# Performance work log

Measured on AMD Instinct MI355X. Metric: run time of the kernel, lower is better.

## Reference

```python
import jax, jax.numpy as jnp
import numpy as np

N_NODES = 100000
N_EDGES = 1600000
IN_F, HID_F, OUT_F = 128, 128, 64


def _sage_conv(x, src, dst, W_self, W_neigh, b, n_nodes):
    # DGL SAGEConv 'mean': out = x @ W_self + mean_{u in N(v)} x_u @ W_neigh + b
    agg = jax.ops.segment_sum(x[src], dst, num_segments=n_nodes)  # [N, d]
    deg = jax.ops.segment_sum(jnp.ones_like(dst, dtype=x.dtype), dst, num_segments=n_nodes)
    neigh = agg / jnp.maximum(deg, 1.0)[:, None]  # zero-in-degree nodes -> 0
    return x @ W_self + neigh @ W_neigh + b


def setup_inputs() -> dict:
    key = jax.random.key(0)
    ks = jax.random.split(key, 8)
    return {
        "features": jax.random.normal(ks[0], (N_NODES, IN_F), dtype=jnp.float32),
        "edge_src": jax.random.randint(ks[1], (N_EDGES,), 0, N_NODES, dtype=jnp.int32),
        "edge_dst": jax.random.randint(ks[2], (N_EDGES,), 0, N_NODES, dtype=jnp.int32),
        "W1_self": jax.random.normal(ks[3], (IN_F, HID_F), dtype=jnp.float32) / np.sqrt(IN_F),
        "W1_neigh": jax.random.normal(ks[4], (IN_F, HID_F), dtype=jnp.float32) / np.sqrt(IN_F),
        "b1": jnp.zeros((HID_F,), dtype=jnp.float32),
        "W2_self": jax.random.normal(ks[5], (HID_F, OUT_F), dtype=jnp.float32) / np.sqrt(HID_F),
        "W2_neigh": jax.random.normal(ks[6], (HID_F, OUT_F), dtype=jnp.float32) / np.sqrt(HID_F),
        "b2": jnp.zeros((OUT_F,), dtype=jnp.float32),
    }


def reference(features, edge_src, edge_dst, W1_self, W1_neigh, b1, W2_self, W2_neigh, b2):
    n = features.shape[0]
    x = _sage_conv(features, edge_src, edge_dst, W1_self, W1_neigh, b1, n)
    x = jax.nn.relu(x)
    # dropout with training=False is a no-op
    return _sage_conv(x, edge_src, edge_dst, W2_self, W2_neigh, b2, n)
```

## Files before the change

kernel.cpp:

```cpp
#include <hip/hip_runtime.h>

#define NODES 100000
#define EDGES 1600000
#define BSH 8
#define NBUCK ((NODES + 255) >> BSH)
#define CHUNK 4096
#define LMAX 8192
#define MCHUNKS ((NODES + 31) / 32)
#define CONVB 12500

using bf16x8 = __attribute__((ext_vector_type(8))) short;
using f32x4  = __attribute__((ext_vector_type(4))) float;
using f32x2  = __attribute__((ext_vector_type(2))) float;

__device__ __forceinline__ unsigned short f2b(float f) {
    unsigned u = __builtin_bit_cast(unsigned, f);
    unsigned r = (u + 0x7FFFu + ((u >> 16) & 1u)) >> 16;
    return (unsigned short)r;
}

__device__ __forceinline__ f32x2 pkadd(f32x2 a, f32x2 b) {
    f32x2 d;
    asm("v_pk_add_f32 %0, %1, %2" : "=v"(d) : "v"(a), "v"(b));
    return d;
}
__device__ __forceinline__ f32x2 pkfma(f32x2 a, f32x2 b, f32x2 c) {
    f32x2 d;
    asm("v_pk_fma_f32 %0, %1, %2, %3" : "=v"(d) : "v"(a), "v"(b), "v"(c));
    return d;
}
__device__ __forceinline__ unsigned cvt2bf(float lo, float hi) {
    unsigned r;
    asm("v_cvt_pk_bf16_f32 %0, %1, %2" : "=v"(r) : "v"(lo), "v"(hi));
    return r;
}

__device__ __forceinline__ void addpk8(f32x2* a, uint2 v) {
    a[0] = pkadd(a[0], __builtin_amdgcn_cvt_pk_f32_fp8((int)v.x, false));
    a[1] = pkadd(a[1], __builtin_amdgcn_cvt_pk_f32_fp8((int)v.x, true));
    a[2] = pkadd(a[2], __builtin_amdgcn_cvt_pk_f32_fp8((int)v.y, false));
    a[3] = pkadd(a[3], __builtin_amdgcn_cvt_pk_f32_fp8((int)v.y, true));
}


__global__ __launch_bounds__(256) void conv_hist(
    const float* __restrict__ in, unsigned short* __restrict__ outb,
    unsigned char* __restrict__ outq, int n4,
    const float* __restrict__ W1s, const float* __restrict__ W1n,
    const float* __restrict__ W2s, const float* __restrict__ W2n,
    unsigned short* __restrict__ Wt1s, unsigned short* __restrict__ Wt1n,
    unsigned short* __restrict__ Wt2s, unsigned short* __restrict__ Wt2n,
    const int* __restrict__ dst, int* __restrict__ bucket_cnt) {
    int t = threadIdx.x;
    if (blockIdx.x < CONVB) {
        int i = blockIdx.x * 256 + t;
        if (i < n4) {
            float4 v = reinterpret_cast<const float4*>(in)[i];
            uint2 o;
            o.x = (unsigned)f2b(v.x) | ((unsigned)f2b(v.y) << 16);
            o.y = (unsigned)f2b(v.z) | ((unsigned)f2b(v.w) << 16);
            reinterpret_cast<uint2*>(outb)[i] = o;
            int pk = __builtin_amdgcn_cvt_pk_fp8_f32(v.x, v.y, 0, false);
            pk = __builtin_amdgcn_cvt_pk_fp8_f32(v.z, v.w, pk, true);
            reinterpret_cast<unsigned*>(outq)[i] = (unsigned)pk;
        }
        if (i < 16384) {
            int k = i >> 7, n = i & 127;
            Wt1s[n * 128 + k] = f2b(W1s[i]);
            Wt1n[n * 128 + k] = f2b(W1n[i]);
        }
        if (i < 8192) {
            int k = i >> 6, n = i & 63;
            Wt2s[n * 128 + k] = f2b(W2s[i]);
            Wt2n[n * 128 + k] = f2b(W2n[i]);
        }
        return;
    }
    __shared__ int lcnt[512];
    lcnt[t] = 0; lcnt[t + 256] = 0;
    __syncthreads();
    int base = (blockIdx.x - CONVB) * 16384;
    int n = EDGES - base;
    if (n > 16384) n = 16384;
    const int4* d4 = reinterpret_cast<const int4*>(dst + base);
    for (int i = t; i < (n >> 2); i += 256) {
        int4 d = d4[i];
        atomicAdd(&lcnt[d.x >> BSH], 1);
        atomicAdd(&lcnt[d.y >> BSH], 1);
        atomicAdd(&lcnt[d.z >> BSH], 1);
        atomicAdd(&lcnt[d.w >> BSH], 1);
    }
    for (int i = (n & ~3) + t; i < n; i += 256) atomicAdd(&lcnt[dst[base + i] >> BSH], 1);
    __syncthreads();
    if (lcnt[t]) atomicAdd(&bucket_cnt[t], lcnt[t]);
    if (lcnt[t + 256]) atomicAdd(&bucket_cnt[t + 256], lcnt[t + 256]);
}

__global__ void bscan_kernel(const int* __restrict__ bucket_cnt, int* __restrict__ bucket_off,
                             int* __restrict__ gcursor, int* __restrict__ row_ptr) {
    __shared__ int sh[512];
    int t = threadIdx.x;
    int v = (t < NBUCK) ? bucket_cnt[t] : 0;
    sh[t] = v;
    __syncthreads();
    for (int off = 1; off < 512; off <<= 1) {
        int x = (t >= off) ? sh[t - off] : 0;
        __syncthreads();
        sh[t] += x;
        __syncthreads();
    }
    int excl = sh[t] - v;
    if (t < NBUCK) { bucket_off[t] = excl; gcursor[t] = excl; }
    if (t == NBUCK) bucket_off[t] = EDGES;
    if (t == 0) row_ptr[NODES] = EDGES;
}

__global__ __launch_bounds__(256) void binscat_kernel(
    const int* __restrict__ src, const int* __restrict__ dst,
    int* __restrict__ gcursor, unsigned* __restrict__ pairs) {
    __shared__ int cnt[512];
    __shared__ int scn[512];
    __shared__ int gbs[512];
    __shared__ int cur[512];
    __shared__ uint2 stage[CHUNK];
    int t = threadIdx.x;
    int base = blockIdx.x * CHUNK;
    int n = EDGES - base;
    if (n > CHUNK) n = CHUNK;

    cnt[t] = 0; cnt[t + 256] = 0;
    __syncthreads();

    uint2 my[16];
#pragma unroll
    for (int i = 0; i < 16; ++i) {
        int idx = t + i * 256;
        if (idx < n) {
            int d = dst[base + idx];
            int s = src[base + idx];
            my[i] = make_uint2((unsigned)d, (unsigned)s);
            atomicAdd(&cnt[d >> BSH], 1);
        } else {
            my[i] = make_uint2(0xFFFFFFFFu, 0);
        }
    }
    __syncthreads();
    scn[t] = cnt[t]; scn[t + 256] = cnt[t + 256];
    __syncthreads();
    for (int off = 1; off < 512; off <<= 1) {
        int a0 = (t >= off) ? scn[t - off] : 0;
        int a1 = (t + 256 >= off) ? scn[t + 256 - off] : 0;
        __syncthreads();
        scn[t] += a0; scn[t + 256] += a1;
        __syncthreads();
    }
    cur[t] = scn[t] - cnt[t];
    cur[t + 256] = scn[t + 256] - cnt[t + 256];
    __syncthreads();
#pragma unroll
    for (int i = 0; i < 16; ++i) {
        if (my[i].x != 0xFFFFFFFFu) {
            int b = (int)(my[i].x >> BSH);
            int p = atomicAdd(&cur[b], 1);
            stage[p] = my[i];
        }
    }
    for (int b2 = t; b2 < 512; b2 += 256) {
        int c = cnt[b2];
        gbs[b2] = (c > 0 && b2 < NBUCK) ? atomicAdd(&gcursor[b2], c) : 0;
    }
    __syncthreads();
    for (int idx = t; idx < n; idx += 256) {
        uint2 p = stage[idx];
        int b = (int)(p.x >> BSH);
        int excl = scn[b] - cnt[b];
        pairs[gbs[b] + idx - excl] = ((p.x & 255u) << 24) | p.y;
    }
}

__global__ __launch_bounds__(256) void localsort_kernel(
    const unsigned* __restrict__ pairs, const int* __restrict__ bucket_off,
    int* __restrict__ row_ptr, int* __restrict__ src_sorted) {
    __shared__ int cnt[256];
    __shared__ int cur[256];
    __shared__ int stage[LMAX];
    int b = blockIdx.x;
    int t = threadIdx.x;
    int node0 = b << BSH;
    int pbeg = bucket_off[b], pend = bucket_off[b + 1];
    int n = pend - pbeg;
    cnt[t] = 0;
    __syncthreads();
    for (int e = pbeg + t; e < pend; e += 256)
        atomicAdd(&cnt[(int)(pairs[e] >> 24)], 1);
    __syncthreads();
    int v = cnt[t];
    cur[t] = v;
    __syncthreads();
    for (int off = 1; off < 256; off <<= 1) {
        int x = (t >= off) ? cur[t - off] : 0;
        __syncthreads();
        cur[t] += x;
        __syncthreads();
    }
    int excl = cur[t] - v;
    int node = node0 + t;
    if (node < NODES) row_ptr[node] = pbeg + excl;
    cur[t] = excl;
    __syncthreads();
    if (n <= LMAX) {
        for (int e = pbeg + t; e < pend; e += 256) {
            unsigned p = pairs[e];
            int pos = atomicAdd(&cur[(int)(p >> 24)], 1);
            stage[pos] = (int)(p & 0xFFFFFFu);
        }
        __syncthreads();
        for (int i = t; i < n; i += 256) src_sorted[pbeg + i] = stage[i];
    } else {
        for (int e = pbeg + t; e < pend; e += 256) {
            unsigned p = pairs[e];
            int pos = atomicAdd(&cur[(int)(p >> 24)], 1);
            src_sorted[pbeg + pos] = (int)(p & 0xFFFFFFu);
        }
    }
}


__global__ __launch_bounds__(256) void agg128_fp8(
    const unsigned char* __restrict__ xq, const int* __restrict__ row_ptr,
    const int* __restrict__ srcs, unsigned short* __restrict__ out) {
    int wave = (blockIdx.x * 256 + threadIdx.x) >> 6;
    int lane = threadIdx.x & 63;
    int sl = lane & 15;
    int n = wave * 4 + (lane >> 4);
    if (n >= NODES) return;
    int beg = row_ptr[n], end = row_ptr[n + 1];
    int gb = lane & 48;

    f32x2 A0[4], A1[4];
#pragma unroll
    for (int i = 0; i < 4; ++i) { A0[i] = {0.f, 0.f}; A1[i] = {0.f, 0.f}; }

    const unsigned char* xs = xq + sl * 8;
    for (int base = beg; base < end; base += 16) {
        int idx = base + sl;
        int sv = (idx < end) ? srcs[idx] : NODES;
        uint2 vv[8], ww[8];
#pragma unroll
        for (int j = 0; j < 8; ++j) {
            int s = __shfl(sv, gb + j, 64);
            vv[j] = *reinterpret_cast<const uint2*>(xs + (size_t)s * 128);
        }
#pragma unroll
        for (int j = 0; j < 8; ++j) {
            int s = __shfl(sv, gb + 8 + j, 64);
            ww[j] = *reinterpret_cast<const uint2*>(xs + (size_t)s * 128);
        }
#pragma unroll
        for (int j = 0; j < 8; ++j) addpk8((j & 1) ? A1 : A0, vv[j]);
#pragma unroll
        for (int j = 0; j < 8; ++j) addpk8((j & 1) ? A0 : A1, ww[j]);
    }

    float inv = 1.0f / fmaxf((float)(end - beg), 1.0f);
    f32x2 iv = {inv, inv};
    f32x2 z = {0.f, 0.f};
    f32x2 r0 = pkfma(pkadd(A0[0], A1[0]), iv, z);
    f32x2 r1 = pkfma(pkadd(A0[1], A1[1]), iv, z);
    f32x2 r2 = pkfma(pkadd(A0[2], A1[2]), iv, z);
    f32x2 r3 = pkfma(pkadd(A0[3], A1[3]), iv, z);
    uint4 o;
    o.x = cvt2bf(r0[0], r0[1]);
    o.y = cvt2bf(r1[0], r1[1]);
    o.z = cvt2bf(r2[0], r2[1]);
    o.w = cvt2bf(r3[0], r3[1]);
    *reinterpret_cast<uint4*>(out + (size_t)n * 128 + sl * 8) = o;
}

__global__ __launch_bounds__(256) void agg64_add8(
    const unsigned char* __restrict__ xq, const int* __restrict__ row_ptr,
    const int* __restrict__ srcs, float* __restrict__ out) {
    int wave = (blockIdx.x * 256 + threadIdx.x) >> 6;
    int lane = threadIdx.x & 63;
    int sl = lane & 7;
    int n = wave * 8 + (lane >> 3);
    if (n >= NODES) return;
    int beg = row_ptr[n], end = row_ptr[n + 1];
    int gb = lane & 56;

    f32x2 A0[4], A1[4];
#pragma unroll
    for (int i = 0; i < 4; ++i) { A0[i] = {0.f, 0.f}; A1[i] = {0.f, 0.f}; }

    const unsigned char* xs = xq + sl * 8;
    for (int base = beg; base < end; base += 8) {
        int idx = base + sl;
        int sv = (idx < end) ? srcs[idx] : NODES;
        uint2 vv[8];
#pragma unroll
        for (int j = 0; j < 8; ++j) {
            int s = __shfl(sv, gb + j, 64);
            vv[j] = *reinterpret_cast<const uint2*>(xs + (size_t)s * 64);
        }
#pragma unroll
        for (int j = 0; j < 8; ++j) addpk8((j & 1) ? A1 : A0, vv[j]);
    }

    float inv = 1.0f / fmaxf((float)(end - beg), 1.0f);
    f32x2 iv = {inv, inv};
    float* op = out + (size_t)n * 64 + sl * 8;
    f32x2 r0 = *reinterpret_cast<f32x2*>(op);
    f32x2 r1 = *reinterpret_cast<f32x2*>(op + 2);
    f32x2 r2 = *reinterpret_cast<f32x2*>(op + 4);
    f32x2 r3 = *reinterpret_cast<f32x2*>(op + 6);
    r0 = pkfma(pkadd(A0[0], A1[0]), iv, r0);
    r1 = pkfma(pkadd(A0[1], A1[1]), iv, r1);
    r2 = pkfma(pkadd(A0[2], A1[2]), iv, r2);
    r3 = pkfma(pkadd(A0[3], A1[3]), iv, r3);
    *reinterpret_cast<f32x2*>(op) = r0;
    *reinterpret_cast<f32x2*>(op + 2) = r1;
    *reinterpret_cast<f32x2*>(op + 4) = r2;
    *reinterpret_cast<f32x2*>(op + 6) = r3;
}


__global__ __launch_bounds__(256, 2) void fused_mlp(
    const unsigned short* __restrict__ featb, const unsigned short* __restrict__ agg,
    const unsigned short* __restrict__ Wt1s, const unsigned short* __restrict__ Wt1n,
    const float* __restrict__ b1, const unsigned short* __restrict__ Wt2s,
    const unsigned short* __restrict__ Wt2n, const float* __restrict__ b2,
    unsigned char* __restrict__ x1h8, float* __restrict__ outp) {
    __shared__ __align__(16) unsigned short x1t[2][32 * 136];
    int wid = threadIdx.x >> 6, lane = threadIdx.x & 63;
    int l15 = lane & 15, quad = lane >> 4;

    bf16x8 B1s[2][4], B1n[2][4];
#pragma unroll
    for (int nt = 0; nt < 2; ++nt) {
        int col = wid * 32 + nt * 16 + l15;
#pragma unroll
        for (int k = 0; k < 4; ++k) {
            B1s[nt][k] = *reinterpret_cast<const bf16x8*>(Wt1s + (size_t)col * 128 + k * 32 + quad * 8);
            B1n[nt][k] = *reinterpret_cast<const bf16x8*>(Wt1n + (size_t)col * 128 + k * 32 + quad * 8);
        }
    }
    bf16x8 B2s[4], B2n[4];
    int col2 = wid * 16 + l15;
#pragma unroll
    for (int k = 0; k < 4; ++k) {
        B2s[k] = *reinterpret_cast<const bf16x8*>(Wt2s + (size_t)col2 * 128 + k * 32 + quad * 8);
        B2n[k] = *reinterpret_cast<const bf16x8*>(Wt2n + (size_t)col2 * 128 + k * 32 + quad * 8);
    }
    float bv1[2];
    bv1[0] = b1[wid * 32 + l15];
    bv1[1] = b1[wid * 32 + 16 + l15];
    float bv2 = b2[col2];

    auto loadA = [&](int cc, bf16x8 (&Afd)[2][4], bf16x8 (&Aad)[2][4]) {
#pragma unroll
        for (int rg = 0; rg < 2; ++rg) {
            int r = cc * 32 + rg * 16 + l15;
            if (r >= NODES) r = NODES - 1;
            const unsigned short* fp = featb + (size_t)r * 128 + quad * 8;
            const unsigned short* ap = agg + (size_t)r * 128 + quad * 8;
#pragma unroll
            for (int k = 0; k < 4; ++k) {
                Afd[rg][k] = *reinterpret_cast<const bf16x8*>(fp + k * 32);
                Aad[rg][k] = *reinterpret_cast<const bf16x8*>(ap + k * 32);
            }
        }
    };

    bf16x8 Af[2][4], Aa[2][4];
    int c = blockIdx.x;
    if (c < MCHUNKS) loadA(c, Af, Aa);
    int buf = 0;
    for (; c < MCHUNKS; c += gridDim.x) {
        int rbase = c * 32;
        int cn = c + (int)gridDim.x;

        f32x4 acc[2][2];
#pragma unroll
        for (int rg = 0; rg < 2; ++rg)
#pragma unroll
            for (int nt = 0; nt < 2; ++nt) acc[rg][nt] = {0.f, 0.f, 0.f, 0.f};
#pragma unroll
        for (int k = 0; k < 4; ++k)
#pragma unroll
            for (int nt = 0; nt < 2; ++nt)
#pragma unroll
                for (int rg = 0; rg < 2; ++rg) {
                    acc[rg][nt] = __builtin_amdgcn_mfma_f32_16x16x32_bf16(Af[rg][k], B1s[nt][k], acc[rg][nt], 0, 0, 0);
                    acc[rg][nt] = __builtin_amdgcn_mfma_f32_16x16x32_bf16(Aa[rg][k], B1n[nt][k], acc[rg][nt], 0, 0, 0);
                }

        bf16x8 Pf[2][4], Pa[2][4];
        if (cn < MCHUNKS) loadA(cn, Pf, Pa);

#pragma unroll
        for (int nt = 0; nt < 2; ++nt)
#pragma unroll
            for (int rg = 0; rg < 2; ++rg)
#pragma unroll
                for (int rr = 0; rr < 4; ++rr) {
                    float v = fmaxf(acc[rg][nt][rr] + bv1[nt], 0.f);
                    x1t[buf][(rg * 16 + quad * 4 + rr) * 136 + wid * 32 + nt * 16 + l15] = f2b(v);
                }
        __syncthreads();

        f32x4 acc2s[2], acc2n[2];
#pragma unroll
        for (int rg = 0; rg < 2; ++rg) { acc2s[rg] = {0.f, 0.f, 0.f, 0.f}; acc2n[rg] = {0.f, 0.f, 0.f, 0.f}; }
#pragma unroll
        for (int k = 0; k < 4; ++k)
#pragma unroll
            for (int rg = 0; rg < 2; ++rg) {
                bf16x8 a = *reinterpret_cast<const bf16x8*>(&x1t[buf][(rg * 16 + l15) * 136 + k * 32 + quad * 8]);
                acc2s[rg] = __builtin_amdgcn_mfma_f32_16x16x32_bf16(a, B2s[k], acc2s[rg], 0, 0, 0);
                acc2n[rg] = __builtin_amdgcn_mfma_f32_16x16x32_bf16(a, B2n[k], acc2n[rg], 0, 0, 0);
            }
#pragma unroll
        for (int rg = 0; rg < 2; ++rg)
#pragma unroll
            for (int rr = 0; rr < 4; ++rr) {
                int row = rbase + rg * 16 + quad * 4 + rr;
                if (row < NODES) {
                    float vn = acc2n[rg][rr];
                    int pk = __builtin_amdgcn_cvt_pk_fp8_f32(vn, vn, 0, false);
                    x1h8[(size_t)row * 64 + col2] = (unsigned char)(pk & 0xFF);
                    outp[(size_t)row * 64 + col2] = acc2s[rg][rr] + bv2;
                }
            }

        buf ^= 1;
        if (cn < MCHUNKS) {
#pragma unroll
            for (int rg = 0; rg < 2; ++rg)
#pragma unroll
                for (int k = 0; k < 4; ++k) {
                    Af[rg][k] = Pf[rg][k];
                    Aa[rg][k] = Pa[rg][k];
                }
        }
    }
}


extern "C" void kernel_launch(void* const* d_in, const int* in_sizes, int n_in,
                              void* d_out, int out_size, void* d_ws, size_t ws_size,
                              hipStream_t stream) {
    const float* features = (const float*)d_in[0];
    const int* esrc = (const int*)d_in[1];
    const int* edst = (const int*)d_in[2];
    const float* W1s = (const float*)d_in[3];
    const float* W1n = (const float*)d_in[4];
    const float* b1  = (const float*)d_in[5];
    const float* W2s = (const float*)d_in[6];
    const float* W2n = (const float*)d_in[7];
    const float* b2  = (const float*)d_in[8];
    float* out = (float*)d_out;

    char* ws = (char*)d_ws;
    size_t off = 0;
    auto alloc = [&](size_t bytes) {
        void* p = ws + off;
        off += (bytes + 255) & ~(size_t)255;
        return p;
    };
    int* bucket_cnt = (int*)alloc(512 * 4);
    int* bucket_off = (int*)alloc(512 * 4);
    int* gcursor    = (int*)alloc(512 * 4);
    int* row_ptr    = (int*)alloc((size_t)(NODES + 1) * 4);
    int* src_sorted = (int*)alloc((size_t)EDGES * 4);
    unsigned* pairs = (unsigned*)alloc((size_t)EDGES * 4);
    unsigned short* featb = (unsigned short*)alloc((size_t)NODES * 128 * 2);
    unsigned char*  feat8 = (unsigned char*)alloc((size_t)(NODES + 1) * 128);
    unsigned short* agg1  = (unsigned short*)alloc((size_t)NODES * 128 * 2);
    unsigned char*  x1h8  = (unsigned char*)alloc((size_t)(NODES + 1) * 64);
    unsigned short* Wt1s  = (unsigned short*)alloc(16384 * 2);
    unsigned short* Wt1n  = (unsigned short*)alloc(16384 * 2);
    unsigned short* Wt2s  = (unsigned short*)alloc(8192 * 2);
    unsigned short* Wt2n  = (unsigned short*)alloc(8192 * 2);

    hipMemsetAsync(bucket_cnt, 0, 512 * 4, stream);
    hipMemsetAsync(feat8 + (size_t)NODES * 128, 0, 128, stream);
    hipMemsetAsync(x1h8 + (size_t)NODES * 64, 0, 64, stream);

    conv_hist<<<CONVB + (EDGES + 16383) / 16384, 256, 0, stream>>>(
        features, featb, feat8, NODES * 128 / 4, W1s, W1n, W2s, W2n,
        Wt1s, Wt1n, Wt2s, Wt2n, edst, bucket_cnt);

    bscan_kernel<<<1, 512, 0, stream>>>(bucket_cnt, bucket_off, gcursor, row_ptr);
    binscat_kernel<<<(EDGES + CHUNK - 1) / CHUNK, 256, 0, stream>>>(esrc, edst, gcursor, pairs);
    localsort_kernel<<<NBUCK, 256, 0, stream>>>(pairs, bucket_off, row_ptr, src_sorted);

    agg128_fp8<<<(NODES / 4 * 64 + 255) / 256, 256, 0, stream>>>(feat8, row_ptr, src_sorted, agg1);

    fused_mlp<<<1024, 256, 0, stream>>>(featb, agg1, Wt1s, Wt1n, b1, Wt2s, Wt2n, b2, x1h8, out);

    agg64_add8<<<(NODES / 8 * 64 + 255) / 256, 256, 0, stream>>>(x1h8, row_ptr, src_sorted, out);
}
```

Measured before the change: 259.2 us.

## Replace persistent prefetching MLP kernel with one block per 32-row chunk

The fused MLP kernel no longer runs as a persistent grid of 1024 blocks that loop over chunks with register prefetch and a double-buffered LDS tile. It now launches one block per 32-row chunk, loads that chunk's operands once, and uses a single LDS buffer. The launch-bounds occupancy hint is dropped. This removes loop overhead and gives the compiler more registers, relying on many resident blocks rather than explicit prefetch to hide memory latency. Each block now reloads the weight fragments, and 3125 blocks are launched instead of 1024.

```diff
diff --git a/kernel.cpp b/kernel.cpp
--- a/kernel.cpp
+++ b/kernel.cpp
@@ -324,15 +324,30 @@
 }
 
 
-__global__ __launch_bounds__(256, 2) void fused_mlp(
+__global__ __launch_bounds__(256) void fused_mlp(
     const unsigned short* __restrict__ featb, const unsigned short* __restrict__ agg,
     const unsigned short* __restrict__ Wt1s, const unsigned short* __restrict__ Wt1n,
     const float* __restrict__ b1, const unsigned short* __restrict__ Wt2s,
     const unsigned short* __restrict__ Wt2n, const float* __restrict__ b2,
     unsigned char* __restrict__ x1h8, float* __restrict__ outp) {
-    __shared__ __align__(16) unsigned short x1t[2][32 * 136];
+    __shared__ __align__(16) unsigned short x1t[32 * 136];
     int wid = threadIdx.x >> 6, lane = threadIdx.x & 63;
     int l15 = lane & 15, quad = lane >> 4;
+    int rbase = blockIdx.x * 32;
+
+    bf16x8 Af[2][4], Aa[2][4];
+#pragma unroll
+    for (int rg = 0; rg < 2; ++rg) {
+        int r = rbase + rg * 16 + l15;
+        if (r >= NODES) r = NODES - 1;
+        const unsigned short* fp = featb + (size_t)r * 128 + quad * 8;
+        const unsigned short* ap = agg + (size_t)r * 128 + quad * 8;
+#pragma unroll
+        for (int k = 0; k < 4; ++k) {
+            Af[rg][k] = *reinterpret_cast<const bf16x8*>(fp + k * 32);
+            Aa[rg][k] = *reinterpret_cast<const bf16x8*>(ap + k * 32);
+        }
+    }
 
     bf16x8 B1s[2][4], B1n[2][4];
 #pragma unroll
@@ -356,93 +371,55 @@
     bv1[1] = b1[wid * 32 + 16 + l15];
     float bv2 = b2[col2];
 
-    auto loadA = [&](int cc, bf16x8 (&Afd)[2][4], bf16x8 (&Aad)[2][4]) {
+    f32x4 acc[2][2];
+#pragma unroll
+    for (int rg = 0; rg < 2; ++rg)
+#pragma unroll
+        for (int nt = 0; nt < 2; ++nt) acc[rg][nt] = {0.f, 0.f, 0.f, 0.f};
+#pragma unroll
+    for (int k = 0; k < 4; ++k)
+#pragma unroll
+        for (int nt = 0; nt < 2; ++nt)
+#pragma unroll
+            for (int rg = 0; rg < 2; ++rg) {
+                acc[rg][nt] = __builtin_amdgcn_mfma_f32_16x16x32_bf16(Af[rg][k], B1s[nt][k], acc[rg][nt], 0, 0, 0);
+                acc[rg][nt] = __builtin_amdgcn_mfma_f32_16x16x32_bf16(Aa[rg][k], B1n[nt][k], acc[rg][nt], 0, 0, 0);
+            }
+
+#pragma unroll
+    for (int nt = 0; nt < 2; ++nt)
+#pragma unroll
+        for (int rg = 0; rg < 2; ++rg)
+#pragma unroll
+            for (int rr = 0; rr < 4; ++rr) {
+                float v = fmaxf(acc[rg][nt][rr] + bv1[nt], 0.f);
+                x1t[(rg * 16 + quad * 4 + rr) * 136 + wid * 32 + nt * 16 + l15] = f2b(v);
+            }
+    __syncthreads();
+
+    f32x4 acc2s[2], acc2n[2];
+#pragma unroll
+    for (int rg = 0; rg < 2; ++rg) { acc2s[rg] = {0.f, 0.f, 0.f, 0.f}; acc2n[rg] = {0.f, 0.f, 0.f, 0.f}; }
+#pragma unroll
+    for (int k = 0; k < 4; ++k)
 #pragma unroll
         for (int rg = 0; rg < 2; ++rg) {
-            int r = cc * 32 + rg * 16 + l15;
-            if (r >= NODES) r = NODES - 1;
-            const unsigned short* fp = featb + (size_t)r * 128 + quad * 8;
-            const unsigned short* ap = agg + (size_t)r * 128 + quad * 8;
-#pragma unroll
-            for (int k = 0; k < 4; ++k) {
-                Afd[rg][k] = *reinterpret_cast<const bf16x8*>(fp + k * 32);
-                Aad[rg][k] = *reinterpret_cast<const bf16x8*>(ap + k * 32);
+            bf16x8 a = *reinterpret_cast<const bf16x8*>(&x1t[(rg * 16 + l15) * 136 + k * 32 + quad * 8]);
+            acc2s[rg] = __builtin_amdgcn_mfma_f32_16x16x32_bf16(a, B2s[k], acc2s[rg], 0, 0, 0);
+            acc2n[rg] = __builtin_amdgcn_mfma_f32_16x16x32_bf16(a, B2n[k], acc2n[rg], 0, 0, 0);
+        }
+#pragma unroll
+    for (int rg = 0; rg < 2; ++rg)
+#pragma unroll
+        for (int rr = 0; rr < 4; ++rr) {
+            int row = rbase + rg * 16 + quad * 4 + rr;
+            if (row < NODES) {
+                float vn = acc2n[rg][rr];
+                int pk = __builtin_amdgcn_cvt_pk_fp8_f32(vn, vn, 0, false);
+                x1h8[(size_t)row * 64 + col2] = (unsigned char)(pk & 0xFF);
+                outp[(size_t)row * 64 + col2] = acc2s[rg][rr] + bv2;
             }
         }
-    };
-
-    bf16x8 Af[2][4], Aa[2][4];
-    int c = blockIdx.x;
-    if (c < MCHUNKS) loadA(c, Af, Aa);
-    int buf = 0;
-    for (; c < MCHUNKS; c += gridDim.x) {
-        int rbase = c * 32;
-        int cn = c + (int)gridDim.x;
-
-        f32x4 acc[2][2];
-#pragma unroll
-        for (int rg = 0; rg < 2; ++rg)
-#pragma unroll
-            for (int nt = 0; nt < 2; ++nt) acc[rg][nt] = {0.f, 0.f, 0.f, 0.f};
-#pragma unroll
-        for (int k = 0; k < 4; ++k)
-#pragma unroll
-            for (int nt = 0; nt < 2; ++nt)
-#pragma unroll
-                for (int rg = 0; rg < 2; ++rg) {
-                    acc[rg][nt] = __builtin_amdgcn_mfma_f32_16x16x32_bf16(Af[rg][k], B1s[nt][k], acc[rg][nt], 0, 0, 0);
-                    acc[rg][nt] = __builtin_amdgcn_mfma_f32_16x16x32_bf16(Aa[rg][k], B1n[nt][k], acc[rg][nt], 0, 0, 0);
-                }
-
-        bf16x8 Pf[2][4], Pa[2][4];
-        if (cn < MCHUNKS) loadA(cn, Pf, Pa);
-
-#pragma unroll
-        for (int nt = 0; nt < 2; ++nt)
-#pragma unroll
-            for (int rg = 0; rg < 2; ++rg)
-#pragma unroll
-                for (int rr = 0; rr < 4; ++rr) {
-                    float v = fmaxf(acc[rg][nt][rr] + bv1[nt], 0.f);
-                    x1t[buf][(rg * 16 + quad * 4 + rr) * 136 + wid * 32 + nt * 16 + l15] = f2b(v);
-                }
-        __syncthreads();
-
-        f32x4 acc2s[2], acc2n[2];
-#pragma unroll
-        for (int rg = 0; rg < 2; ++rg) { acc2s[rg] = {0.f, 0.f, 0.f, 0.f}; acc2n[rg] = {0.f, 0.f, 0.f, 0.f}; }
-#pragma unroll
-        for (int k = 0; k < 4; ++k)
-#pragma unroll
-            for (int rg = 0; rg < 2; ++rg) {
-                bf16x8 a = *reinterpret_cast<const bf16x8*>(&x1t[buf][(rg * 16 + l15) * 136 + k * 32 + quad * 8]);
-                acc2s[rg] = __builtin_amdgcn_mfma_f32_16x16x32_bf16(a, B2s[k], acc2s[rg], 0, 0, 0);
-                acc2n[rg] = __builtin_amdgcn_mfma_f32_16x16x32_bf16(a, B2n[k], acc2n[rg], 0, 0, 0);
-            }
-#pragma unroll
-        for (int rg = 0; rg < 2; ++rg)
-#pragma unroll
-            for (int rr = 0; rr < 4; ++rr) {
-                int row = rbase + rg * 16 + quad * 4 + rr;
-                if (row < NODES) {
-                    float vn = acc2n[rg][rr];
-                    int pk = __builtin_amdgcn_cvt_pk_fp8_f32(vn, vn, 0, false);
-                    x1h8[(size_t)row * 64 + col2] = (unsigned char)(pk & 0xFF);
-                    outp[(size_t)row * 64 + col2] = acc2s[rg][rr] + bv2;
-                }
-            }
-
-        buf ^= 1;
-        if (cn < MCHUNKS) {
-#pragma unroll
-            for (int rg = 0; rg < 2; ++rg)
-#pragma unroll
-                for (int k = 0; k < 4; ++k) {
-                    Af[rg][k] = Pf[rg][k];
-                    Aa[rg][k] = Pa[rg][k];
-                }
-        }
-    }
 }
 
 
@@ -496,7 +473,7 @@
 
     agg128_fp8<<<(NODES / 4 * 64 + 255) / 256, 256, 0, stream>>>(feat8, row_ptr, src_sorted, agg1);
 
-    fused_mlp<<<1024, 256, 0, stream>>>(featb, agg1, Wt1s, Wt1n, b1, Wt2s, Wt2n, b2, x1h8, out);
+    fused_mlp<<<MCHUNKS, 256, 0, stream>>>(featb, agg1, Wt1s, Wt1n, b1, Wt2s, Wt2n, b2, x1h8, out);
 
     agg64_add8<<<(NODES / 8 * 64 + 255) / 256, 256, 0, stream>>>(x1h8, row_ptr, src_sorted, out);
 }
```

Result: slower. 280.0 us (+8.0%).

## Stage layer-1 weights in swizzled LDS instead of registers in fused MLP

Applied to the files above, without the earlier changes.

Moves the layer-1 self/neighbor weight fragments out of per-thread registers into a 64KB XOR-swizzled shared-memory tile loaded once per block, and reads them per k-step inside the loop. This frees VGPRs and halves the grid to 512 blocks with a fixed stride. x1t becomes single-buffered with an extra barrier, and the row bounds clamps and guards are removed. The removed guards rely on NODES being a multiple of 32, and the extra LDS reads and barrier add per-chunk latency.

```diff
diff --git a/kernel.cpp b/kernel.cpp
--- a/kernel.cpp
+++ b/kernel.cpp
@@ -8,6 +8,7 @@
 #define LMAX 8192
 #define MCHUNKS ((NODES + 31) / 32)
 #define CONVB 12500
+#define MLPGRID 512
 
 using bf16x8 = __attribute__((ext_vector_type(8))) short;
 using f32x4  = __attribute__((ext_vector_type(4))) float;
@@ -32,6 +33,12 @@
 __device__ __forceinline__ unsigned cvt2bf(float lo, float hi) {
     unsigned r;
     asm("v_cvt_pk_bf16_f32 %0, %1, %2" : "=v"(r) : "v"(lo), "v"(hi));
+    return r;
+}
+
+__device__ __forceinline__ bf16x8 gl16(const unsigned short* p) {
+    bf16x8 r;
+    asm volatile("global_load_dwordx4 %0, %1, off" : "=&v"(r) : "v"(p));
     return r;
 }
 
@@ -330,26 +337,31 @@
     const float* __restrict__ b1, const unsigned short* __restrict__ Wt2s,
     const unsigned short* __restrict__ Wt2n, const float* __restrict__ b2,
     unsigned char* __restrict__ x1h8, float* __restrict__ outp) {
-    __shared__ __align__(16) unsigned short x1t[2][32 * 136];
+    __shared__ __align__(16) unsigned short w1t[32768];
+    __shared__ __align__(16) unsigned short x1t[32 * 136];
     int wid = threadIdx.x >> 6, lane = threadIdx.x & 63;
     int l15 = lane & 15, quad = lane >> 4;
 
-    bf16x8 B1s[2][4], B1n[2][4];
-#pragma unroll
-    for (int nt = 0; nt < 2; ++nt) {
-        int col = wid * 32 + nt * 16 + l15;
-#pragma unroll
-        for (int k = 0; k < 4; ++k) {
-            B1s[nt][k] = *reinterpret_cast<const bf16x8*>(Wt1s + (size_t)col * 128 + k * 32 + quad * 8);
-            B1n[nt][k] = *reinterpret_cast<const bf16x8*>(Wt1n + (size_t)col * 128 + k * 32 + quad * 8);
-        }
-    }
+    {
+        const uint4* gs = reinterpret_cast<const uint4*>(Wt1s);
+        const uint4* gn = reinterpret_cast<const uint4*>(Wt1n);
+        uint4* ls = reinterpret_cast<uint4*>(w1t);
+        uint4* ln = reinterpret_cast<uint4*>(w1t) + 2048;
+#pragma unroll
+        for (int i = 0; i < 8; ++i) {
+            int g = threadIdx.x + i * 256;
+            int sw = (g & ~15) | ((g & 15) ^ ((g >> 4) & 7));
+            ls[sw] = gs[g];
+            ln[sw] = gn[g];
+        }
+    }
+
+    int col2 = wid * 16 + l15;
     bf16x8 B2s[4], B2n[4];
-    int col2 = wid * 16 + l15;
 #pragma unroll
     for (int k = 0; k < 4; ++k) {
-        B2s[k] = *reinterpret_cast<const bf16x8*>(Wt2s + (size_t)col2 * 128 + k * 32 + quad * 8);
-        B2n[k] = *reinterpret_cast<const bf16x8*>(Wt2n + (size_t)col2 * 128 + k * 32 + quad * 8);
+        B2s[k] = gl16(Wt2s + (size_t)col2 * 128 + k * 32 + quad * 8);
+        B2n[k] = gl16(Wt2n + (size_t)col2 * 128 + k * 32 + quad * 8);
     }
     float bv1[2];
     bv1[0] = b1[wid * 32 + l15];
@@ -360,7 +372,6 @@
 #pragma unroll
         for (int rg = 0; rg < 2; ++rg) {
             int r = cc * 32 + rg * 16 + l15;
-            if (r >= NODES) r = NODES - 1;
             const unsigned short* fp = featb + (size_t)r * 128 + quad * 8;
             const unsigned short* ap = agg + (size_t)r * 128 + quad * 8;
 #pragma unroll
@@ -374,10 +385,18 @@
     bf16x8 Af[2][4], Aa[2][4];
     int c = blockIdx.x;
     if (c < MCHUNKS) loadA(c, Af, Aa);
-    int buf = 0;
-    for (; c < MCHUNKS; c += gridDim.x) {
+
+    asm volatile("s_waitcnt vmcnt(0)" ::: "memory");
+    __builtin_amdgcn_sched_barrier(0);
+    __syncthreads();
+
+    int swz = l15 & 7;
+    const unsigned short* wb0 = w1t + (size_t)(wid * 32 + l15) * 128;
+    const unsigned short* wb1 = w1t + (size_t)(wid * 32 + 16 + l15) * 128;
+
+    for (; c < MCHUNKS; c += MLPGRID) {
         int rbase = c * 32;
-        int cn = c + (int)gridDim.x;
+        int cn = c + MLPGRID;
 
         f32x4 acc[2][2];
 #pragma unroll
@@ -385,14 +404,20 @@
 #pragma unroll
             for (int nt = 0; nt < 2; ++nt) acc[rg][nt] = {0.f, 0.f, 0.f, 0.f};
 #pragma unroll
-        for (int k = 0; k < 4; ++k)
-#pragma unroll
-            for (int nt = 0; nt < 2; ++nt)
-#pragma unroll
-                for (int rg = 0; rg < 2; ++rg) {
-                    acc[rg][nt] = __builtin_amdgcn_mfma_f32_16x16x32_bf16(Af[rg][k], B1s[nt][k], acc[rg][nt], 0, 0, 0);
-                    acc[rg][nt] = __builtin_amdgcn_mfma_f32_16x16x32_bf16(Aa[rg][k], B1n[nt][k], acc[rg][nt], 0, 0, 0);
-                }
+        for (int k = 0; k < 4; ++k) {
+            int so = ((k * 4 + quad) ^ swz) << 3;
+            bf16x8 b1s0 = *reinterpret_cast<const bf16x8*>(wb0 + so);
+            bf16x8 b1n0 = *reinterpret_cast<const bf16x8*>(wb0 + 16384 + so);
+            bf16x8 b1s1 = *reinterpret_cast<const bf16x8*>(wb1 + so);
+            bf16x8 b1n1 = *reinterpret_cast<const bf16x8*>(wb1 + 16384 + so);
+#pragma unroll
+            for (int rg = 0; rg < 2; ++rg) {
+                acc[rg][0] = __builtin_amdgcn_mfma_f32_16x16x32_bf16(Af[rg][k], b1s0, acc[rg][0], 0, 0, 0);
+                acc[rg][0] = __builtin_amdgcn_mfma_f32_16x16x32_bf16(Aa[rg][k], b1n0, acc[rg][0], 0, 0, 0);
+                acc[rg][1] = __builtin_amdgcn_mfma_f32_16x16x32_bf16(Af[rg][k], b1s1, acc[rg][1], 0, 0, 0);
+                acc[rg][1] = __builtin_amdgcn_mfma_f32_16x16x32_bf16(Aa[rg][k], b1n1, acc[rg][1], 0, 0, 0);
+            }
+        }
 
         bf16x8 Pf[2][4], Pa[2][4];
         if (cn < MCHUNKS) loadA(cn, Pf, Pa);
@@ -404,7 +429,7 @@
 #pragma unroll
                 for (int rr = 0; rr < 4; ++rr) {
                     float v = fmaxf(acc[rg][nt][rr] + bv1[nt], 0.f);
-                    x1t[buf][(rg * 16 + quad * 4 + rr) * 136 + wid * 32 + nt * 16 + l15] = f2b(v);
+                    x1t[(rg * 16 + quad * 4 + rr) * 136 + wid * 32 + nt * 16 + l15] = f2b(v);
                 }
         __syncthreads();
 
@@ -415,24 +440,23 @@
         for (int k = 0; k < 4; ++k)
 #pragma unroll
             for (int rg = 0; rg < 2; ++rg) {
-                bf16x8 a = *reinterpret_cast<const bf16x8*>(&x1t[buf][(rg * 16 + l15) * 136 + k * 32 + quad * 8]);
+                bf16x8 a = *reinterpret_cast<const bf16x8*>(&x1t[(rg * 16 + l15) * 136 + k * 32 + quad * 8]);
                 acc2s[rg] = __builtin_amdgcn_mfma_f32_16x16x32_bf16(a, B2s[k], acc2s[rg], 0, 0, 0);
                 acc2n[rg] = __builtin_amdgcn_mfma_f32_16x16x32_bf16(a, B2n[k], acc2n[rg], 0, 0, 0);
             }
+        __syncthreads();
+
 #pragma unroll
         for (int rg = 0; rg < 2; ++rg)
 #pragma unroll
             for (int rr = 0; rr < 4; ++rr) {
                 int row = rbase + rg * 16 + quad * 4 + rr;
-                if (row < NODES) {
-                    float vn = acc2n[rg][rr];
-                    int pk = __builtin_amdgcn_cvt_pk_fp8_f32(vn, vn, 0, false);
-                    x1h8[(size_t)row * 64 + col2] = (unsigned char)(pk & 0xFF);
-                    outp[(size_t)row * 64 + col2] = acc2s[rg][rr] + bv2;
-                }
+                float vn = acc2n[rg][rr];
+                int pk = __builtin_amdgcn_cvt_pk_fp8_f32(vn, vn, 0, false);
+                x1h8[(size_t)row * 64 + col2] = (unsigned char)(pk & 0xFF);
+                outp[(size_t)row * 64 + col2] = acc2s[rg][rr] + bv2;
             }
 
-        buf ^= 1;
         if (cn < MCHUNKS) {
 #pragma unroll
             for (int rg = 0; rg < 2; ++rg)
@@ -496,7 +520,7 @@
 
     agg128_fp8<<<(NODES / 4 * 64 + 255) / 256, 256, 0, stream>>>(feat8, row_ptr, src_sorted, agg1);
 
-    fused_mlp<<<1024, 256, 0, stream>>>(featb, agg1, Wt1s, Wt1n, b1, Wt2s, Wt2n, b2, x1h8, out);
+    fused_mlp<<<MLPGRID, 256, 0, stream>>>(featb, agg1, Wt1s, Wt1n, b1, Wt2s, Wt2n, b2, x1h8, out);
 
     agg64_add8<<<(NODES / 8 * 64 + 255) / 256, 256, 0, stream>>>(x1h8, row_ptr, src_sorted, out);
 }
```

After: 255.8 us. Within noise of the previous version (-1.3%).
